# Optimization experiments

Hardware: AMD Instinct MI355X
Metric: run time of the kernel (lower is better)

The kernel has to match this reference:

```python
import jax, jax.numpy as jnp
import numpy as np

B, S, D = 4, 2048, 512
H, HD, RL = 8, 64, 64   # nheads, head_dim = D//H, rl_dim
TEMPER = 1.0
BETA = 1.0
SLOPE = 0.01  # LeakyReLU negative slope
LN_EPS = 1e-5


def setup_inputs() -> dict:
    key = jax.random.key(0)
    ks = jax.random.split(key, 12)
    scale = 0.02
    return {
        "h":   jax.random.normal(ks[0], (B, S, D), dtype=jnp.float32),
        "rh":  jax.random.normal(ks[1], (B, S, RL), dtype=jnp.float32),
        "Wl":  jax.random.normal(ks[2], (D, D), dtype=jnp.float32) * scale,   # linear_l (in,out)
        "Wr":  jax.random.normal(ks[3], (D, D), dtype=jnp.float32) * scale,   # linear_r
        "al":  jax.random.normal(ks[4], (HD,), dtype=jnp.float32) * scale,    # att_l: Linear(head_dim,1)
        "ar":  jax.random.normal(ks[5], (HD,), dtype=jnp.float32) * scale,    # att_r
        "Wrs": jax.random.normal(ks[6], (RL, RL * H), dtype=jnp.float32) * scale,  # r_source
        "Wrt": jax.random.normal(ks[7], (RL, RL * H), dtype=jnp.float32) * scale,  # r_target
        "Wf":  jax.random.normal(ks[8], (D, D), dtype=jnp.float32) * scale,   # linear_final
        "ln_g": jnp.ones((D,), dtype=jnp.float32),
        "ln_b": jnp.zeros((D,), dtype=jnp.float32),
    }


def _layer_norm(x, g, b):
    mu = jnp.mean(x, axis=-1, keepdims=True)
    var = jnp.mean(jnp.square(x - mu), axis=-1, keepdims=True)
    return (x - mu) * jax.lax.rsqrt(var + LN_EPS) * g + b


def reference(h, rh, Wl, Wr, al, ar, Wrs, Wrt, Wf, ln_g, ln_b):
    leaky = lambda x: jnp.where(x >= 0, x, SLOPE * x)
    # projections -> [B, H, S, HD]
    fl = (h @ Wl).reshape(B, S, H, HD).transpose(0, 2, 1, 3)
    fr = (h @ Wr).reshape(B, S, H, HD).transpose(0, 2, 1, 3)
    # additive attention logits: [B,H,S,1] + [B,H,1,S]
    sl = jnp.einsum('bhsd,d->bhs', leaky(fl), al)
    sr = jnp.einsum('bhsd,d->bhs', leaky(fr), ar)
    score = sl[:, :, :, None] + sr[:, :, None, :]
    # relation-embedding bilinear bias: r_k @ r_q -> [B,H,S,S]
    r_k = (rh @ Wrs).reshape(B, S, H, RL).transpose(0, 2, 1, 3)   # [B,H,S,RL]
    r_q = (rh @ Wrt).reshape(B, S, H, RL).transpose(0, 2, 3, 1)   # [B,H,RL,S]
    score = score + BETA * jnp.einsum('bhsr,bhrt->bhst', r_k, r_q)
    score = jax.nn.softmax(score / TEMPER, axis=-1)
    # context and output projection (dropout = 0 -> identity)
    context = jnp.einsum('bhst,bhtd->bhsd', score, fr)
    h_sa = context.transpose(0, 2, 1, 3).reshape(B, S, H * HD)
    fh = h_sa @ Wf
    return _layer_norm(h + fh, ln_g, ln_b)
```

## Files before the change

### kernel.cpp

```cpp
#include <hip/hip_runtime.h>
#include <math.h>

#define B_ 4
#define S_ 2048
#define D_ 512
#define H_ 8
#define HD_ 64
#define RL_ 64
#define LN_EPS 1e-5f
#define SLOPE 0.01f
#define LOG2E 1.4426950408889634f

typedef __attribute__((ext_vector_type(8))) __bf16 bf16x8;
typedef __attribute__((ext_vector_type(4))) float f32x4;

__device__ __forceinline__ float leaky(float x) { return x >= 0.f ? x : SLOPE * x; }

__device__ __forceinline__ ushort f2bf(float f) {
    union { float f; unsigned u; } v; v.f = f;
    unsigned r = v.u + 0x7fffu + ((v.u >> 16) & 1u);
    return (ushort)(r >> 16);
}
__device__ __forceinline__ unsigned fbits(float f) {
    union { float f; unsigned u; } v; v.f = f; return v.u;
}

__device__ __forceinline__ void g2lds16(const void* g, void* l) {
    __builtin_amdgcn_global_load_lds(
        (const __attribute__((address_space(1))) void*)(uintptr_t)g,
        (__attribute__((address_space(3))) void*)(uintptr_t)l, 16, 0, 0);
}

__global__ __launch_bounds__(256) void prep_cast(
    const float* __restrict__ h, const float* __restrict__ rh,
    ushort* __restrict__ hb, ushort* __restrict__ rhb)
{
    const int bx = blockIdx.x, tid = threadIdx.x;
    const float* in = (bx < 4096) ? h : rh;
    ushort* o = (bx < 4096) ? hb : rhb;
    const int i = (bx < 4096 ? bx : bx - 4096) * 256 + tid;
    const float4 v = ((const float4*)in)[i];
    ushort4 u; u.x = f2bf(v.x); u.y = f2bf(v.y); u.z = f2bf(v.z); u.w = f2bf(v.w);
    ((ushort4*)o)[i] = u;
}

__global__ __launch_bounds__(256) void prep_tr(
    const float* __restrict__ Wr, const float* __restrict__ Wf,
    const float* __restrict__ Wrs, const float* __restrict__ Wrt,
    ushort* __restrict__ WrT, ushort* __restrict__ WfT,
    ushort* __restrict__ WrsT, ushort* __restrict__ WrtT)
{
    __shared__ float TS[64][65];
    int bx = blockIdx.x;
    const float* in; ushort* out; int K, tk, tn;
    if (bx < 64)       { in = Wr;  out = WrT;  K = 512; tk = bx & 7; tn = bx >> 3; }
    else if (bx < 128) { in = Wf;  out = WfT;  K = 512; bx -= 64; tk = bx & 7; tn = bx >> 3; }
    else if (bx < 136) { in = Wrs; out = WrsT; K = 64;  tk = 0; tn = bx - 128; }
    else               { in = Wrt; out = WrtT; K = 64;  tk = 0; tn = bx - 136; }
    const int k0 = tk * 64, n0 = tn * 64;
    const int r = threadIdx.x >> 4, c4 = (threadIdx.x & 15) * 4;
    #pragma unroll
    for (int p = 0; p < 4; ++p) {
        const int row = r + 16 * p;
        const float4 v = *(const float4*)(in + (size_t)(k0 + row) * 512 + n0 + c4);
        TS[row][c4] = v.x; TS[row][c4 + 1] = v.y;
        TS[row][c4 + 2] = v.z; TS[row][c4 + 3] = v.w;
    }
    __syncthreads();
    #pragma unroll
    for (int p = 0; p < 4; ++p) {
        const int nn = r + 16 * p;
        ushort4 o;
        o.x = f2bf(TS[c4 + 0][nn]); o.y = f2bf(TS[c4 + 1][nn]);
        o.z = f2bf(TS[c4 + 2][nn]); o.w = f2bf(TS[c4 + 3][nn]);
        *(ushort4*)(out + (size_t)(n0 + nn) * K + k0 + c4) = o;
    }
}

template <int MODE>
__global__ __launch_bounds__(256) void mfma_gemm(
    const ushort* __restrict__ A, const ushort* __restrict__ WT,
    void* __restrict__ Cout, float* __restrict__ sred,
    const float* __restrict__ avec, int K, float scale,
    const ushort* __restrict__ WT2, void* __restrict__ Cout2, float scale2)
{
    __shared__ ushort As[2][64 * 32];
    __shared__ ushort Bs[2][128 * 32];

    const int tid = threadIdx.x;
    const int lane = tid & 63, w = tid >> 6;
    const int ln = lane & 15, quad = lane >> 4;
    const int wm = w >> 1, wn = w & 1;
    const int m0 = blockIdx.x * 64, n0 = blockIdx.y * 128;

    const ushort* wt = WT; void* co = Cout; float scl = scale;
    if constexpr (MODE == 3) {
        if (blockIdx.z) { wt = WT2; co = Cout2; scl = scale2; }
    }

    const int srA = tid >> 2;
    const int lchA = ((lane & 3) - (srA >> 1)) & 3;
    const ushort* AgB = A + (size_t)(m0 + srA) * K + lchA * 8;
    const int srB = w * 32 + (lane >> 2);
    const int lchB = ((lane & 3) - (srB >> 1)) & 3;
    const ushort* BgB0 = wt + (size_t)(n0 + srB) * K + lchB * 8;
    const ushort* BgB1 = BgB0 + (size_t)16 * K;
    const int aoff = tid * 8;
    const int boff = srB * 32 + (lane & 3) * 8;

    const int pc = (quad + (ln >> 1)) & 3;

    g2lds16(AgB, &As[0][aoff]);
    g2lds16(BgB0, &Bs[0][boff]);
    g2lds16(BgB1, &Bs[0][boff + 512]);

    f32x4 acc[2][4] = {};
    int buf = 0;
    for (int k0 = 0; k0 < K; k0 += 32) {
        __syncthreads();
        if (k0 + 32 < K) {
            g2lds16(AgB + k0 + 32, &As[buf ^ 1][aoff]);
            g2lds16(BgB0 + k0 + 32, &Bs[buf ^ 1][boff]);
            g2lds16(BgB1 + k0 + 32, &Bs[buf ^ 1][boff + 512]);
        }
        bf16x8 af[2], bfr[4];
        #pragma unroll
        for (int mi = 0; mi < 2; ++mi)
            af[mi] = *(const bf16x8*)&As[buf][(wm * 32 + mi * 16 + ln) * 32 + pc * 8];
        #pragma unroll
        for (int ni = 0; ni < 4; ++ni)
            bfr[ni] = *(const bf16x8*)&Bs[buf][(wn * 64 + ni * 16 + ln) * 32 + pc * 8];
        #pragma unroll
        for (int mi = 0; mi < 2; ++mi)
            #pragma unroll
            for (int ni = 0; ni < 4; ++ni)
                acc[mi][ni] = __builtin_amdgcn_mfma_f32_16x16x32_bf16(
                    af[mi], bfr[ni], acc[mi][ni], 0, 0, 0);
        buf ^= 1;
    }

    if constexpr (MODE == 0) {
        float* C = (float*)co;
        #pragma unroll
        for (int mi = 0; mi < 2; ++mi) {
            const int row = m0 + wm * 32 + mi * 16 + quad * 4;
            #pragma unroll
            for (int ni = 0; ni < 4; ++ni) {
                const int col = n0 + wn * 64 + ni * 16 + ln;
                #pragma unroll
                for (int r = 0; r < 4; ++r)
                    C[(size_t)(row + r) * 512 + col] = acc[mi][ni][r];
            }
        }
    }
    if constexpr (MODE == 2 || MODE == 3) {
        const int head = blockIdx.y * 2 + wn;
        const int b = m0 >> 11;
        const size_t bh = (size_t)b * H_ + head;
        if constexpr (MODE == 2) {
            ushort* frT = (ushort*)co;
            #pragma unroll
            for (int mi = 0; mi < 2; ++mi) {
                const int s = (m0 & (S_ - 1)) + wm * 32 + mi * 16 + quad * 4;
                #pragma unroll
                for (int ni = 0; ni < 4; ++ni) {
                    const int d = ni * 16 + ln;
                    ushort4 o;
                    o.x = f2bf(acc[mi][ni][0]); o.y = f2bf(acc[mi][ni][1]);
                    o.z = f2bf(acc[mi][ni][2]); o.w = f2bf(acc[mi][ni][3]);
                    *(ushort4*)(frT + (bh * 64 + d) * S_ + s) = o;
                }
            }
            float a4[4];
            #pragma unroll
            for (int ni = 0; ni < 4; ++ni) a4[ni] = avec[ni * 16 + ln];
            #pragma unroll
            for (int mi = 0; mi < 2; ++mi) {
                const int s = (m0 & (S_ - 1)) + wm * 32 + mi * 16 + quad * 4;
                #pragma unroll
                for (int r = 0; r < 4; ++r) {
                    float v = 0.f;
                    #pragma unroll
                    for (int ni = 0; ni < 4; ++ni)
                        v += leaky(acc[mi][ni][r]) * a4[ni];
                    #pragma unroll
                    for (int off = 8; off; off >>= 1) v += __shfl_xor(v, off, 16);
                    if (ln == 0) sred[bh * S_ + s + r] = v * scl;
                }
            }
        }
        if constexpr (MODE == 3) {
            ushort* O = (ushort*)co;
            #pragma unroll
            for (int mi = 0; mi < 2; ++mi) {
                const int s = (m0 & (S_ - 1)) + wm * 32 + mi * 16 + quad * 4;
                #pragma unroll
                for (int ni = 0; ni < 4; ++ni) {
                    const int d = ni * 16 + ln;
                    #pragma unroll
                    for (int r = 0; r < 4; ++r)
                        O[(bh * S_ + s + r) * 64 + d] = f2bf(acc[mi][ni][r] * scl);
                }
            }
        }
    }
}

__global__ __launch_bounds__(256, 4) void attn_mfma(
    const ushort* __restrict__ frT, const ushort* __restrict__ rk,
    const ushort* __restrict__ rq, const float* __restrict__ sr,
    ushort* __restrict__ hsa)
{
    __shared__ ushort RQ[2][64][64];
    __shared__ ushort FT[2][64][64];
    __shared__ ushort PS[4][16][64];

    const int tid = threadIdx.x;
    const int w = tid >> 6;
    const int lane = tid & 63;
    const int ln = lane & 15;
    const int quad = lane >> 4;
    const int b = blockIdx.z, h = blockIdx.y, q0 = blockIdx.x * 64;
    const size_t bh = (size_t)b * H_ + h;

    const ushort* rkb = rk + ((bh * S_ + q0 + w * 16 + ln) << 6);
    const bf16x8 a0 = *(const bf16x8*)(rkb + quad * 8);
    const bf16x8 a1 = *(const bf16x8*)(rkb + 32 + quad * 8);

    const ushort* rqb = rq + (bh * S_ << 6);
    const ushort* ftb = frT + (size_t)bh * 64 * S_;
    const float* srp = sr + bh * S_;

    const int rl = lane >> 3;
    const int pg = lane & 7;
    const int row_b = w * 16 + rl;
    const int sgF = (pg - rl) & 7;
    const int sgR0 = (pg - 4 * w - (rl >> 2)) & 7;
    const int sgR1 = (pg - 4 * w - 2 - (rl >> 2)) & 7;

    #define STAGE(bf, t0)                                                     \
        {                                                                     \
            g2lds16(rqb + ((size_t)((t0) + row_b) << 6) + sgR0 * 8,           \
                    &RQ[bf][row_b][pg * 8]);                                  \
            g2lds16(rqb + ((size_t)((t0) + row_b + 8) << 6) + sgR1 * 8,       \
                    &RQ[bf][row_b + 8][pg * 8]);                              \
            g2lds16(ftb + (size_t)row_b * S_ + (t0) + sgF * 8,                \
                    &FT[bf][row_b][pg * 8]);                                  \
            g2lds16(ftb + (size_t)(row_b + 8) * S_ + (t0) + sgF * 8,          \
                    &FT[bf][row_b + 8][pg * 8]);                              \
        }

    STAGE(0, 0)
    __syncthreads();

    float lsum[4] = {};
    f32x4 ctx[4] = {};
    int buf = 0;

    for (int t0 = 0; t0 < S_; t0 += 64) {
        if (t0 + 64 < S_) STAGE(buf ^ 1, t0 + 64)
        const float4 srv = *(const float4*)(srp + t0 + 4 * ln);

        f32x4 sc[4];
        #pragma unroll
        for (int jb = 0; jb < 4; ++jb) {
            const int tr = 4 * ln + jb;
            const bf16x8 b0 = *(const bf16x8*)&RQ[buf][tr][((quad + ln) & 7) * 8];
            const bf16x8 b1 = *(const bf16x8*)&RQ[buf][tr][((quad + 4 + ln) & 7) * 8];
            f32x4 t = {0.f, 0.f, 0.f, 0.f};
            t = __builtin_amdgcn_mfma_f32_16x16x32_bf16(a0, b0, t, 0, 0, 0);
            t = __builtin_amdgcn_mfma_f32_16x16x32_bf16(a1, b1, t, 0, 0, 0);
            sc[jb] = t;
        }

        #pragma unroll
        for (int r = 0; r < 4; ++r) {
            const float p0 = __builtin_amdgcn_exp2f(sc[0][r] + srv.x);
            const float p1 = __builtin_amdgcn_exp2f(sc[1][r] + srv.y);
            const float p2 = __builtin_amdgcn_exp2f(sc[2][r] + srv.z);
            const float p3 = __builtin_amdgcn_exp2f(sc[3][r] + srv.w);
            lsum[r] += (p0 + p1) + (p2 + p3);
            const unsigned lo = (fbits(p0) >> 16) | (fbits(p1) & 0xffff0000u);
            const unsigned hi = (fbits(p2) >> 16) | (fbits(p3) & 0xffff0000u);
            const int prow = quad * 4 + r;
            *(uint2*)&PS[w][prow][(((ln >> 1) + prow) & 7) * 8 + (ln & 1) * 4] =
                make_uint2(lo, hi);
        }

        const bf16x8 pa0 = *(const bf16x8*)&PS[w][ln][((quad + ln) & 7) * 8];
        const bf16x8 pa1 = *(const bf16x8*)&PS[w][ln][((quad + 4 + ln) & 7) * 8];
        #pragma unroll
        for (int jb = 0; jb < 4; ++jb) {
            const bf16x8 fb0 = *(const bf16x8*)&FT[buf][16 * jb + ln][((quad + ln) & 7) * 8];
            const bf16x8 fb1 = *(const bf16x8*)&FT[buf][16 * jb + ln][((quad + 4 + ln) & 7) * 8];
            ctx[jb] = __builtin_amdgcn_mfma_f32_16x16x32_bf16(pa0, fb0, ctx[jb], 0, 0, 0);
            ctx[jb] = __builtin_amdgcn_mfma_f32_16x16x32_bf16(pa1, fb1, ctx[jb], 0, 0, 0);
        }

        __syncthreads();
        buf ^= 1;
    }

    #pragma unroll
    for (int r = 0; r < 4; ++r) {
        float l = lsum[r];
        #pragma unroll
        for (int off = 8; off; off >>= 1) l += __shfl_xor(l, off, 16);
        const float inv = 1.f / l;
        const int q = q0 + w * 16 + quad * 4 + r;
        ushort* orow = hsa + (size_t)(b * S_ + q) * D_ + h * 64;
        #pragma unroll
        for (int jb = 0; jb < 4; ++jb)
            orow[16 * jb + ln] = f2bf(ctx[jb][r] * inv);
    }
}

__global__ __launch_bounds__(256) void ln_kernel(
    const float* __restrict__ h, const float* __restrict__ fh,
    const float* __restrict__ g, const float* __restrict__ bb,
    float* __restrict__ out)
{
    const int row = blockIdx.x, tid = threadIdx.x;
    const float* hp = h + (size_t)row * 512;
    const float* fp = fh + (size_t)row * 512;
    const float x0 = hp[tid] + fp[tid];
    const float x1 = hp[tid + 256] + fp[tid + 256];
    __shared__ float red[4];

    float s = x0 + x1;
    #pragma unroll
    for (int off = 32; off; off >>= 1) s += __shfl_xor(s, off, 64);
    if ((tid & 63) == 0) red[tid >> 6] = s;
    __syncthreads();
    const float mu = (red[0] + red[1] + red[2] + red[3]) * (1.f / 512.f);

    const float d0 = x0 - mu, d1 = x1 - mu;
    float v = d0 * d0 + d1 * d1;
    #pragma unroll
    for (int off = 32; off; off >>= 1) v += __shfl_xor(v, off, 64);
    __syncthreads();
    if ((tid & 63) == 0) red[tid >> 6] = v;
    __syncthreads();
    const float var = (red[0] + red[1] + red[2] + red[3]) * (1.f / 512.f);
    const float inv = rsqrtf(var + LN_EPS);

    out[(size_t)row * 512 + tid] = d0 * inv * g[tid] + bb[tid];
    out[(size_t)row * 512 + tid + 256] = d1 * inv * g[tid + 256] + bb[tid + 256];
}

extern "C" void kernel_launch(void* const* d_in, const int* in_sizes, int n_in,
                              void* d_out, int out_size, void* d_ws, size_t ws_size,
                              hipStream_t stream)
{
    const float* h   = (const float*)d_in[0];
    const float* rh  = (const float*)d_in[1];
    const float* Wr  = (const float*)d_in[3];
    const float* ar  = (const float*)d_in[5];
    const float* Wrs = (const float*)d_in[6];
    const float* Wrt = (const float*)d_in[7];
    const float* Wf  = (const float*)d_in[8];
    const float* lng = (const float*)d_in[9];
    const float* lnb = (const float*)d_in[10];
    float* out = (float*)d_out;
    char* wsb  = (char*)d_ws;

    const size_t MB = (size_t)1 << 20;
    ushort* hb   = (ushort*)(wsb);
    ushort* rhb  = (ushort*)(wsb + 8 * MB);
    ushort* WrT  = (ushort*)(wsb + 9 * MB);
    ushort* WfT  = (ushort*)(wsb + 9 * MB + 512 * 1024);
    ushort* WrsT = (ushort*)(wsb + 10 * MB);
    ushort* WrtT = (ushort*)(wsb + 10 * MB + 64 * 1024);
    ushort* frT  = (ushort*)(wsb + 11 * MB);
    ushort* rkw  = (ushort*)(wsb + 19 * MB);
    ushort* rqw  = (ushort*)(wsb + 27 * MB);
    float*  sr   = (float*) (wsb + 35 * MB);
    ushort* hsab = (ushort*)(wsb + 36 * MB);
    float*  fh   = (float*) (wsb + 44 * MB);

    dim3 blk(256);
    prep_cast<<<dim3(4608), blk, 0, stream>>>(h, rh, hb, rhb);
    prep_tr<<<dim3(144), blk, 0, stream>>>(Wr, Wf, Wrs, Wrt, WrT, WfT, WrsT, WrtT);

    dim3 gG(128, 4);
    mfma_gemm<2><<<gG, blk, 0, stream>>>(hb, WrT, frT, sr, ar, 512, LOG2E,
                                         nullptr, nullptr, 0.f);
    mfma_gemm<3><<<dim3(128, 4, 2), blk, 0, stream>>>(
        rhb, WrsT, rkw, nullptr, nullptr, 64, LOG2E, WrtT, rqw, 1.0f);
    attn_mfma<<<dim3(S_ / 64, H_, B_), blk, 0, stream>>>(frT, rkw, rqw, sr, hsab);
    mfma_gemm<0><<<gG, blk, 0, stream>>>(hsab, WfT, fh, nullptr, nullptr, 512, 1.0f,
                                         nullptr, nullptr, 0.f);
    ln_kernel<<<dim3(B_ * S_), blk, 0, stream>>>(h, fh, lng, lnb, out);
}
```

Measured before the change: 184.6 us.

## Merge prep and projection launches, double attention query tile per block

The two prep kernels are merged into one launch, and the fr and rk/rq projection GEMMs are combined into a single three-slice launch. The attention kernel now handles 128 queries per block (two 16-row sub-tiles per wave), so each staged RQ/FT tile is reused across twice as many queries. Each iteration now covers two 64-key halves. This is meant to cut launch overhead and halve the global/LDS traffic for keys and values. In exchange it raises register pressure (launch bounds lowered to 2) and leaves half as many attention blocks to fill the GPU.

```diff
diff --git a/kernel.cpp b/kernel.cpp
--- a/kernel.cpp
+++ b/kernel.cpp
@@ -31,34 +31,33 @@
         (__attribute__((address_space(3))) void*)(uintptr_t)l, 16, 0, 0);
 }
 
-__global__ __launch_bounds__(256) void prep_cast(
+__global__ __launch_bounds__(256) void prep(
     const float* __restrict__ h, const float* __restrict__ rh,
-    ushort* __restrict__ hb, ushort* __restrict__ rhb)
-{
-    const int bx = blockIdx.x, tid = threadIdx.x;
-    const float* in = (bx < 4096) ? h : rh;
-    ushort* o = (bx < 4096) ? hb : rhb;
-    const int i = (bx < 4096 ? bx : bx - 4096) * 256 + tid;
-    const float4 v = ((const float4*)in)[i];
-    ushort4 u; u.x = f2bf(v.x); u.y = f2bf(v.y); u.z = f2bf(v.z); u.w = f2bf(v.w);
-    ((ushort4*)o)[i] = u;
-}
-
-__global__ __launch_bounds__(256) void prep_tr(
     const float* __restrict__ Wr, const float* __restrict__ Wf,
     const float* __restrict__ Wrs, const float* __restrict__ Wrt,
+    ushort* __restrict__ hb, ushort* __restrict__ rhb,
     ushort* __restrict__ WrT, ushort* __restrict__ WfT,
     ushort* __restrict__ WrsT, ushort* __restrict__ WrtT)
 {
+    const int bx = blockIdx.x, tid = threadIdx.x;
+    if (bx < 4608) {
+        const float* in = (bx < 4096) ? h : rh;
+        ushort* o = (bx < 4096) ? hb : rhb;
+        const int i = (bx < 4096 ? bx : bx - 4096) * 256 + tid;
+        const float4 v = ((const float4*)in)[i];
+        ushort4 u; u.x = f2bf(v.x); u.y = f2bf(v.y); u.z = f2bf(v.z); u.w = f2bf(v.w);
+        ((ushort4*)o)[i] = u;
+        return;
+    }
     __shared__ float TS[64][65];
-    int bx = blockIdx.x;
+    int t = bx - 4608;
     const float* in; ushort* out; int K, tk, tn;
-    if (bx < 64)       { in = Wr;  out = WrT;  K = 512; tk = bx & 7; tn = bx >> 3; }
-    else if (bx < 128) { in = Wf;  out = WfT;  K = 512; bx -= 64; tk = bx & 7; tn = bx >> 3; }
-    else if (bx < 136) { in = Wrs; out = WrsT; K = 64;  tk = 0; tn = bx - 128; }
-    else               { in = Wrt; out = WrtT; K = 64;  tk = 0; tn = bx - 136; }
+    if (t < 64)       { in = Wr;  out = WrT;  K = 512; tk = t & 7; tn = t >> 3; }
+    else if (t < 128) { in = Wf;  out = WfT;  K = 512; t -= 64; tk = t & 7; tn = t >> 3; }
+    else if (t < 136) { in = Wrs; out = WrsT; K = 64;  tk = 0; tn = t - 128; }
+    else              { in = Wrt; out = WrtT; K = 64;  tk = 0; tn = t - 136; }
     const int k0 = tk * 64, n0 = tn * 64;
-    const int r = threadIdx.x >> 4, c4 = (threadIdx.x & 15) * 4;
+    const int r = tid >> 4, c4 = (tid & 15) * 4;
     #pragma unroll
     for (int p = 0; p < 4; ++p) {
         const int row = r + 16 * p;
@@ -77,12 +76,12 @@
     }
 }
 
-template <int MODE>
-__global__ __launch_bounds__(256) void mfma_gemm(
-    const ushort* __restrict__ A, const ushort* __restrict__ WT,
-    void* __restrict__ Cout, float* __restrict__ sred,
-    const float* __restrict__ avec, int K, float scale,
-    const ushort* __restrict__ WT2, void* __restrict__ Cout2, float scale2)
+__global__ __launch_bounds__(256) void proj(
+    const ushort* __restrict__ hb, const ushort* __restrict__ rhb,
+    const ushort* __restrict__ WrT, const ushort* __restrict__ WrsT,
+    const ushort* __restrict__ WrtT,
+    ushort* __restrict__ frT, ushort* __restrict__ rkw, ushort* __restrict__ rqw,
+    float* __restrict__ sred, const float* __restrict__ ar)
 {
     __shared__ ushort As[2][64 * 32];
     __shared__ ushort Bs[2][128 * 32];
@@ -92,11 +91,12 @@
     const int ln = lane & 15, quad = lane >> 4;
     const int wm = w >> 1, wn = w & 1;
     const int m0 = blockIdx.x * 64, n0 = blockIdx.y * 128;
-
-    const ushort* wt = WT; void* co = Cout; float scl = scale;
-    if constexpr (MODE == 3) {
-        if (blockIdx.z) { wt = WT2; co = Cout2; scl = scale2; }
-    }
+    const int z = blockIdx.z;
+
+    const ushort* A; const ushort* wt; ushort* co; float scl; int K;
+    if (z == 0)      { A = hb;  wt = WrT;  co = frT; scl = LOG2E; K = 512; }
+    else if (z == 1) { A = rhb; wt = WrsT; co = rkw; scl = LOG2E; K = 64; }
+    else             { A = rhb; wt = WrtT; co = rqw; scl = 1.0f;  K = 64; }
 
     const int srA = tid >> 2;
     const int lchA = ((lane & 3) - (srA >> 1)) & 3;
@@ -107,7 +107,6 @@
     const ushort* BgB1 = BgB0 + (size_t)16 * K;
     const int aoff = tid * 8;
     const int boff = srB * 32 + (lane & 3) * 8;
-
     const int pc = (quad + (ln >> 1)) & 3;
 
     g2lds16(AgB, &As[0][aoff]);
@@ -139,96 +138,81 @@
         buf ^= 1;
     }
 
-    if constexpr (MODE == 0) {
-        float* C = (float*)co;
+    const int head = blockIdx.y * 2 + wn;
+    const int b = m0 >> 11;
+    const size_t bh = (size_t)b * H_ + head;
+    if (z == 0) {
         #pragma unroll
         for (int mi = 0; mi < 2; ++mi) {
-            const int row = m0 + wm * 32 + mi * 16 + quad * 4;
+            const int s = (m0 & (S_ - 1)) + wm * 32 + mi * 16 + quad * 4;
             #pragma unroll
             for (int ni = 0; ni < 4; ++ni) {
-                const int col = n0 + wn * 64 + ni * 16 + ln;
+                const int d = ni * 16 + ln;
+                ushort4 o;
+                o.x = f2bf(acc[mi][ni][0]); o.y = f2bf(acc[mi][ni][1]);
+                o.z = f2bf(acc[mi][ni][2]); o.w = f2bf(acc[mi][ni][3]);
+                *(ushort4*)(co + (bh * 64 + d) * S_ + s) = o;
+            }
+        }
+        float a4[4];
+        #pragma unroll
+        for (int ni = 0; ni < 4; ++ni) a4[ni] = ar[ni * 16 + ln];
+        #pragma unroll
+        for (int mi = 0; mi < 2; ++mi) {
+            const int s = (m0 & (S_ - 1)) + wm * 32 + mi * 16 + quad * 4;
+            #pragma unroll
+            for (int r = 0; r < 4; ++r) {
+                float v = 0.f;
+                #pragma unroll
+                for (int ni = 0; ni < 4; ++ni)
+                    v += leaky(acc[mi][ni][r]) * a4[ni];
+                #pragma unroll
+                for (int off = 8; off; off >>= 1) v += __shfl_xor(v, off, 16);
+                if (ln == 0) sred[bh * S_ + s + r] = v * scl;
+            }
+        }
+    } else {
+        #pragma unroll
+        for (int mi = 0; mi < 2; ++mi) {
+            const int s = (m0 & (S_ - 1)) + wm * 32 + mi * 16 + quad * 4;
+            #pragma unroll
+            for (int ni = 0; ni < 4; ++ni) {
+                const int d = ni * 16 + ln;
                 #pragma unroll
                 for (int r = 0; r < 4; ++r)
-                    C[(size_t)(row + r) * 512 + col] = acc[mi][ni][r];
-            }
-        }
-    }
-    if constexpr (MODE == 2 || MODE == 3) {
-        const int head = blockIdx.y * 2 + wn;
-        const int b = m0 >> 11;
-        const size_t bh = (size_t)b * H_ + head;
-        if constexpr (MODE == 2) {
-            ushort* frT = (ushort*)co;
-            #pragma unroll
-            for (int mi = 0; mi < 2; ++mi) {
-                const int s = (m0 & (S_ - 1)) + wm * 32 + mi * 16 + quad * 4;
-                #pragma unroll
-                for (int ni = 0; ni < 4; ++ni) {
-                    const int d = ni * 16 + ln;
-                    ushort4 o;
-                    o.x = f2bf(acc[mi][ni][0]); o.y = f2bf(acc[mi][ni][1]);
-                    o.z = f2bf(acc[mi][ni][2]); o.w = f2bf(acc[mi][ni][3]);
-                    *(ushort4*)(frT + (bh * 64 + d) * S_ + s) = o;
-                }
-            }
-            float a4[4];
-            #pragma unroll
-            for (int ni = 0; ni < 4; ++ni) a4[ni] = avec[ni * 16 + ln];
-            #pragma unroll
-            for (int mi = 0; mi < 2; ++mi) {
-                const int s = (m0 & (S_ - 1)) + wm * 32 + mi * 16 + quad * 4;
-                #pragma unroll
-                for (int r = 0; r < 4; ++r) {
-                    float v = 0.f;
-                    #pragma unroll
-                    for (int ni = 0; ni < 4; ++ni)
-                        v += leaky(acc[mi][ni][r]) * a4[ni];
-                    #pragma unroll
-                    for (int off = 8; off; off >>= 1) v += __shfl_xor(v, off, 16);
-                    if (ln == 0) sred[bh * S_ + s + r] = v * scl;
-                }
-            }
-        }
-        if constexpr (MODE == 3) {
-            ushort* O = (ushort*)co;
-            #pragma unroll
-            for (int mi = 0; mi < 2; ++mi) {
-                const int s = (m0 & (S_ - 1)) + wm * 32 + mi * 16 + quad * 4;
-                #pragma unroll
-                for (int ni = 0; ni < 4; ++ni) {
-                    const int d = ni * 16 + ln;
-                    #pragma unroll
-                    for (int r = 0; r < 4; ++r)
-                        O[(bh * S_ + s + r) * 64 + d] = f2bf(acc[mi][ni][r] * scl);
-                }
-            }
-        }
-    }
-}
-
-__global__ __launch_bounds__(256, 4) void attn_mfma(
+                    co[(bh * S_ + s + r) * 64 + d] = f2bf(acc[mi][ni][r] * scl);
+            }
+        }
+    }
+}
+
+__global__ __launch_bounds__(256, 2) void attn_mfma(
     const ushort* __restrict__ frT, const ushort* __restrict__ rk,
     const ushort* __restrict__ rq, const float* __restrict__ sr,
     ushort* __restrict__ hsa)
 {
     __shared__ ushort RQ[2][64][64];
     __shared__ ushort FT[2][64][64];
-    __shared__ ushort PS[4][16][64];
+    __shared__ ushort PS[8][16][64];
 
     const int tid = threadIdx.x;
     const int w = tid >> 6;
     const int lane = tid & 63;
     const int ln = lane & 15;
     const int quad = lane >> 4;
-    const int b = blockIdx.z, h = blockIdx.y, q0 = blockIdx.x * 64;
+    const int b = blockIdx.z, h = blockIdx.y, q0 = blockIdx.x * 128;
     const size_t bh = (size_t)b * H_ + h;
 
-    const ushort* rkb = rk + ((bh * S_ + q0 + w * 16 + ln) << 6);
-    const bf16x8 a0 = *(const bf16x8*)(rkb + quad * 8);
-    const bf16x8 a1 = *(const bf16x8*)(rkb + 32 + quad * 8);
-
-    const ushort* rqb = rq + (bh * S_ << 6);
-    const ushort* ftb = frT + (size_t)bh * 64 * S_;
+    bf16x8 a[2][2];
+    #pragma unroll
+    for (int qs = 0; qs < 2; ++qs) {
+        const ushort* p = rk + ((bh * S_ + q0 + 32 * w + 16 * qs + ln) << 6);
+        a[qs][0] = *(const bf16x8*)(p + quad * 8);
+        a[qs][1] = *(const bf16x8*)(p + 32 + quad * 8);
+    }
+
+    const ushort* rq_g = rq + (bh * S_ << 6);
+    const ushort* ft_g = frT + (size_t)bh * 64 * S_;
     const float* srp = sr + bh * S_;
 
     const int rl = lane >> 3;
@@ -238,80 +222,175 @@
     const int sgR0 = (pg - 4 * w - (rl >> 2)) & 7;
     const int sgR1 = (pg - 4 * w - 2 - (rl >> 2)) & 7;
 
-    #define STAGE(bf, t0)                                                     \
+    #define STAGE(BUF, t0)                                                    \
         {                                                                     \
-            g2lds16(rqb + ((size_t)((t0) + row_b) << 6) + sgR0 * 8,           \
-                    &RQ[bf][row_b][pg * 8]);                                  \
-            g2lds16(rqb + ((size_t)((t0) + row_b + 8) << 6) + sgR1 * 8,       \
-                    &RQ[bf][row_b + 8][pg * 8]);                              \
-            g2lds16(ftb + (size_t)row_b * S_ + (t0) + sgF * 8,                \
-                    &FT[bf][row_b][pg * 8]);                                  \
-            g2lds16(ftb + (size_t)(row_b + 8) * S_ + (t0) + sgF * 8,          \
-                    &FT[bf][row_b + 8][pg * 8]);                              \
-        }
+            g2lds16(rq_g + ((size_t)((t0) + row_b) << 6) + sgR0 * 8,          \
+                    &RQ[BUF][row_b][pg * 8]);                                 \
+            g2lds16(rq_g + ((size_t)((t0) + row_b + 8) << 6) + sgR1 * 8,      \
+                    &RQ[BUF][row_b + 8][pg * 8]);                             \
+            g2lds16(ft_g + (size_t)row_b * S_ + (t0) + sgF * 8,               \
+                    &FT[BUF][row_b][pg * 8]);                                 \
+            g2lds16(ft_g + (size_t)(row_b + 8) * S_ + (t0) + sgF * 8,         \
+                    &FT[BUF][row_b + 8][pg * 8]);                             \
+        }
+
+    const ushort* rqrA = &RQ[0][0][0] + 4 * ln * 64 + ((quad + ln) & 7) * 8;
+    const ushort* rqrB = &RQ[0][0][0] + 4 * ln * 64 + ((quad + 4 + ln) & 7) * 8;
+    const ushort* ftrA = &FT[0][0][0] + ln * 64 + ((quad + ln) & 7) * 8;
+    const ushort* ftrB = &FT[0][0][0] + ln * 64 + ((quad + 4 + ln) & 7) * 8;
+    ushort* sb[2];
+    sb[0] = &PS[w * 2][0][0]; sb[1] = &PS[w * 2 + 1][0][0];
+    int wr_off[4];
+    #pragma unroll
+    for (int r = 0; r < 4; ++r) {
+        const int prow = quad * 4 + r;
+        wr_off[r] = prow * 64 + (((ln >> 1) + prow) & 7) * 8 + (ln & 1) * 4;
+    }
+    const int rd0 = ln * 64 + ((quad + ln) & 7) * 8;
+    const int rd1 = ln * 64 + ((quad + 4 + ln) & 7) * 8;
 
     STAGE(0, 0)
     __syncthreads();
 
-    float lsum[4] = {};
-    f32x4 ctx[4] = {};
+    float lsum[2][4] = {};
+    f32x4 ctx[2][4] = {};
+
+    for (int t0 = 0; t0 < S_; t0 += 128) {
+        #pragma unroll
+        for (int half = 0; half < 2; ++half) {
+            const int tc = t0 + 64 * half;
+            if (tc + 64 < S_) {
+                if (half == 0) STAGE(1, tc + 64)
+                else           STAGE(0, tc + 64)
+            }
+            const float4 srv = *(const float4*)(srp + tc + 4 * ln);
+
+            f32x4 sc[2][4];
+            #pragma unroll
+            for (int jb = 0; jb < 4; ++jb) {
+                const bf16x8 b0 = *(const bf16x8*)(rqrA + half * 4096 + jb * 64);
+                const bf16x8 b1 = *(const bf16x8*)(rqrB + half * 4096 + jb * 64);
+                #pragma unroll
+                for (int qs = 0; qs < 2; ++qs) {
+                    f32x4 t = {0.f, 0.f, 0.f, 0.f};
+                    t = __builtin_amdgcn_mfma_f32_16x16x32_bf16(a[qs][0], b0, t, 0, 0, 0);
+                    t = __builtin_amdgcn_mfma_f32_16x16x32_bf16(a[qs][1], b1, t, 0, 0, 0);
+                    sc[qs][jb] = t;
+                }
+            }
+
+            #pragma unroll
+            for (int qs = 0; qs < 2; ++qs)
+                #pragma unroll
+                for (int r = 0; r < 4; ++r) {
+                    const float p0 = __builtin_amdgcn_exp2f(sc[qs][0][r] + srv.x);
+                    const float p1 = __builtin_amdgcn_exp2f(sc[qs][1][r] + srv.y);
+                    const float p2 = __builtin_amdgcn_exp2f(sc[qs][2][r] + srv.z);
+                    const float p3 = __builtin_amdgcn_exp2f(sc[qs][3][r] + srv.w);
+                    lsum[qs][r] += (p0 + p1) + (p2 + p3);
+                    const unsigned lo = (fbits(p0) >> 16) | (fbits(p1) & 0xffff0000u);
+                    const unsigned hi = (fbits(p2) >> 16) | (fbits(p3) & 0xffff0000u);
+                    *(uint2*)(sb[qs] + wr_off[r]) = make_uint2(lo, hi);
+                }
+
+            const bf16x8 pa00 = *(const bf16x8*)(sb[0] + rd0);
+            const bf16x8 pa01 = *(const bf16x8*)(sb[0] + rd1);
+            const bf16x8 pa10 = *(const bf16x8*)(sb[1] + rd0);
+            const bf16x8 pa11 = *(const bf16x8*)(sb[1] + rd1);
+            #pragma unroll
+            for (int jb = 0; jb < 4; ++jb) {
+                const bf16x8 fb0 = *(const bf16x8*)(ftrA + half * 4096 + jb * 1024);
+                const bf16x8 fb1 = *(const bf16x8*)(ftrB + half * 4096 + jb * 1024);
+                ctx[0][jb] = __builtin_amdgcn_mfma_f32_16x16x32_bf16(pa00, fb0, ctx[0][jb], 0, 0, 0);
+                ctx[0][jb] = __builtin_amdgcn_mfma_f32_16x16x32_bf16(pa01, fb1, ctx[0][jb], 0, 0, 0);
+                ctx[1][jb] = __builtin_amdgcn_mfma_f32_16x16x32_bf16(pa10, fb0, ctx[1][jb], 0, 0, 0);
+                ctx[1][jb] = __builtin_amdgcn_mfma_f32_16x16x32_bf16(pa11, fb1, ctx[1][jb], 0, 0, 0);
+            }
+
+            __syncthreads();
+        }
+    }
+
+    #pragma unroll
+    for (int qs = 0; qs < 2; ++qs)
+        #pragma unroll
+        for (int r = 0; r < 4; ++r) {
+            float l = lsum[qs][r];
+            #pragma unroll
+            for (int off = 8; off; off >>= 1) l += __shfl_xor(l, off, 16);
+            const float inv = 1.f / l;
+            const int q = q0 + 32 * w + 16 * qs + quad * 4 + r;
+            ushort* orow = hsa + (size_t)(b * S_ + q) * D_ + h * 64;
+            #pragma unroll
+            for (int jb = 0; jb < 4; ++jb)
+                orow[16 * jb + ln] = f2bf(ctx[qs][jb][r] * inv);
+        }
+}
+
+__global__ __launch_bounds__(256) void gemm_out(
+    const ushort* __restrict__ A, const ushort* __restrict__ WT,
+    float* __restrict__ C)
+{
+    __shared__ ushort As[2][64 * 32];
+    __shared__ ushort Bs[2][128 * 32];
+
+    const int tid = threadIdx.x;
+    const int lane = tid & 63, w = tid >> 6;
+    const int ln = lane & 15, quad = lane >> 4;
+    const int wm = w >> 1, wn = w & 1;
+    const int m0 = blockIdx.x * 64, n0 = blockIdx.y * 128;
+    const int K = 512;
+
+    const int srA = tid >> 2;
+    const int lchA = ((lane & 3) - (srA >> 1)) & 3;
+    const ushort* AgB = A + (size_t)(m0 + srA) * K + lchA * 8;
+    const int srB = w * 32 + (lane >> 2);
+    const int lchB = ((lane & 3) - (srB >> 1)) & 3;
+    const ushort* BgB0 = WT + (size_t)(n0 + srB) * K + lchB * 8;
+    const ushort* BgB1 = BgB0 + (size_t)16 * K;
+    const int aoff = tid * 8;
+    const int boff = srB * 32 + (lane & 3) * 8;
+    const int pc = (quad + (ln >> 1)) & 3;
+
+    g2lds16(AgB, &As[0][aoff]);
+    g2lds16(BgB0, &Bs[0][boff]);
+    g2lds16(BgB1, &Bs[0][boff + 512]);
+
+    f32x4 acc[2][4] = {};
     int buf = 0;
-
-    for (int t0 = 0; t0 < S_; t0 += 64) {
-        if (t0 + 64 < S_) STAGE(buf ^ 1, t0 + 64)
-        const float4 srv = *(const float4*)(srp + t0 + 4 * ln);
-
-        f32x4 sc[4];
-        #pragma unroll
-        for (int jb = 0; jb < 4; ++jb) {
-            const int tr = 4 * ln + jb;
-            const bf16x8 b0 = *(const bf16x8*)&RQ[buf][tr][((quad + ln) & 7) * 8];
-            const bf16x8 b1 = *(const bf16x8*)&RQ[buf][tr][((quad + 4 + ln) & 7) * 8];
-            f32x4 t = {0.f, 0.f, 0.f, 0.f};
-            t = __builtin_amdgcn_mfma_f32_16x16x32_bf16(a0, b0, t, 0, 0, 0);
-            t = __builtin_amdgcn_mfma_f32_16x16x32_bf16(a1, b1, t, 0, 0, 0);
-            sc[jb] = t;
-        }
-
-        #pragma unroll
-        for (int r = 0; r < 4; ++r) {
-            const float p0 = __builtin_amdgcn_exp2f(sc[0][r] + srv.x);
-            const float p1 = __builtin_amdgcn_exp2f(sc[1][r] + srv.y);
-            const float p2 = __builtin_amdgcn_exp2f(sc[2][r] + srv.z);
-            const float p3 = __builtin_amdgcn_exp2f(sc[3][r] + srv.w);
-            lsum[r] += (p0 + p1) + (p2 + p3);
-            const unsigned lo = (fbits(p0) >> 16) | (fbits(p1) & 0xffff0000u);
-            const unsigned hi = (fbits(p2) >> 16) | (fbits(p3) & 0xffff0000u);
-            const int prow = quad * 4 + r;
-            *(uint2*)&PS[w][prow][(((ln >> 1) + prow) & 7) * 8 + (ln & 1) * 4] =
-                make_uint2(lo, hi);
-        }
-
-        const bf16x8 pa0 = *(const bf16x8*)&PS[w][ln][((quad + ln) & 7) * 8];
-        const bf16x8 pa1 = *(const bf16x8*)&PS[w][ln][((quad + 4 + ln) & 7) * 8];
-        #pragma unroll
-        for (int jb = 0; jb < 4; ++jb) {
-            const bf16x8 fb0 = *(const bf16x8*)&FT[buf][16 * jb + ln][((quad + ln) & 7) * 8];
-            const bf16x8 fb1 = *(const bf16x8*)&FT[buf][16 * jb + ln][((quad + 4 + ln) & 7) * 8];
-            ctx[jb] = __builtin_amdgcn_mfma_f32_16x16x32_bf16(pa0, fb0, ctx[jb], 0, 0, 0);
-            ctx[jb] = __builtin_amdgcn_mfma_f32_16x16x32_bf16(pa1, fb1, ctx[jb], 0, 0, 0);
-        }
-
+    for (int k0 = 0; k0 < K; k0 += 32) {
         __syncthreads();
+        if (k0 + 32 < K) {
+            g2lds16(AgB + k0 + 32, &As[buf ^ 1][aoff]);
+            g2lds16(BgB0 + k0 + 32, &Bs[buf ^ 1][boff]);
+            g2lds16(BgB1 + k0 + 32, &Bs[buf ^ 1][boff + 512]);
+        }
+        bf16x8 af[2], bfr[4];
+        #pragma unroll
+        for (int mi = 0; mi < 2; ++mi)
+            af[mi] = *(const bf16x8*)&As[buf][(wm * 32 + mi * 16 + ln) * 32 + pc * 8];
+        #pragma unroll
+        for (int ni = 0; ni < 4; ++ni)
+            bfr[ni] = *(const bf16x8*)&Bs[buf][(wn * 64 + ni * 16 + ln) * 32 + pc * 8];
+        #pragma unroll
+        for (int mi = 0; mi < 2; ++mi)
+            #pragma unroll
+            for (int ni = 0; ni < 4; ++ni)
+                acc[mi][ni] = __builtin_amdgcn_mfma_f32_16x16x32_bf16(
+                    af[mi], bfr[ni], acc[mi][ni], 0, 0, 0);
         buf ^= 1;
     }
 
     #pragma unroll
-    for (int r = 0; r < 4; ++r) {
-        float l = lsum[r];
-        #pragma unroll
-        for (int off = 8; off; off >>= 1) l += __shfl_xor(l, off, 16);
-        const float inv = 1.f / l;
-        const int q = q0 + w * 16 + quad * 4 + r;
-        ushort* orow = hsa + (size_t)(b * S_ + q) * D_ + h * 64;
-        #pragma unroll
-        for (int jb = 0; jb < 4; ++jb)
-            orow[16 * jb + ln] = f2bf(ctx[jb][r] * inv);
+    for (int mi = 0; mi < 2; ++mi) {
+        const int row = m0 + wm * 32 + mi * 16 + quad * 4;
+        #pragma unroll
+        for (int ni = 0; ni < 4; ++ni) {
+            const int col = n0 + wn * 64 + ni * 16 + ln;
+            #pragma unroll
+            for (int r = 0; r < 4; ++r)
+                C[(size_t)(row + r) * 512 + col] = acc[mi][ni][r];
+        }
     }
 }
 
@@ -379,16 +458,11 @@
     float*  fh   = (float*) (wsb + 44 * MB);
 
     dim3 blk(256);
-    prep_cast<<<dim3(4608), blk, 0, stream>>>(h, rh, hb, rhb);
-    prep_tr<<<dim3(144), blk, 0, stream>>>(Wr, Wf, Wrs, Wrt, WrT, WfT, WrsT, WrtT);
-
-    dim3 gG(128, 4);
-    mfma_gemm<2><<<gG, blk, 0, stream>>>(hb, WrT, frT, sr, ar, 512, LOG2E,
-                                         nullptr, nullptr, 0.f);
-    mfma_gemm<3><<<dim3(128, 4, 2), blk, 0, stream>>>(
-        rhb, WrsT, rkw, nullptr, nullptr, 64, LOG2E, WrtT, rqw, 1.0f);
-    attn_mfma<<<dim3(S_ / 64, H_, B_), blk, 0, stream>>>(frT, rkw, rqw, sr, hsab);
-    mfma_gemm<0><<<gG, blk, 0, stream>>>(hsab, WfT, fh, nullptr, nullptr, 512, 1.0f,
-                                         nullptr, nullptr, 0.f);
+    prep<<<dim3(4752), blk, 0, stream>>>(h, rh, Wr, Wf, Wrs, Wrt,
+                                         hb, rhb, WrT, WfT, WrsT, WrtT);
+    proj<<<dim3(128, 4, 3), blk, 0, stream>>>(hb, rhb, WrT, WrsT, WrtT,
+                                              frT, rkw, rqw, sr, ar);
+    attn_mfma<<<dim3(S_ / 128, H_, B_), blk, 0, stream>>>(frT, rkw, rqw, sr, hsab);
+    gemm_out<<<dim3(128, 4), blk, 0, stream>>>(hsab, WfT, fh);
     ln_kernel<<<dim3(B_ * S_), blk, 0, stream>>>(h, fh, lng, lnb, out);
 }
```

Result: faster. 175.5 us (-4.9%).
